# Kernel tuning notes

Measured on AMD Instinct MI355X. Metric: run time of the kernel, lower is better.

The kernel has to match this reference:

```python
import jax, jax.numpy as jnp
import numpy as np

B, N, D = 4, 2048, 256
H, DA, DL = 4, 64, 64          # heads, q/k dim per head, u/v dim per head
NUM_BUCKETS = 128
LN_EPS = 1e-5


def _layernorm(x, g, b):
    mu = jnp.mean(x, axis=-1, keepdims=True)
    var = jnp.var(x, axis=-1, keepdims=True)
    return (x - mu) * jax.lax.rsqrt(var + LN_EPS) * g + b


def setup_inputs() -> dict:
    key = jax.random.key(0)
    ks = jax.random.split(key, 8)
    x = jax.random.normal(ks[0], (B, N, D), jnp.float32)
    lengths = jax.random.randint(ks[1], (B,), 1, N + 1).astype(jnp.int64)
    timestamps = jnp.sort(
        jax.random.randint(ks[2], (B, N), 0, 10_000_000), axis=1
    ).astype(jnp.int64)
    F_uvqk = H * (2 * DL + 2 * DA)
    W_uvqk = jax.random.normal(ks[3], (D, F_uvqk), jnp.float32) * 0.02
    b_uvqk = jnp.zeros((F_uvqk,), jnp.float32)
    W_o = jax.random.normal(ks[4], (H * DL, D), jnp.float32) * 0.02
    b_o = jnp.zeros((D,), jnp.float32)
    ln_in_g = jnp.ones((D,), jnp.float32)
    ln_in_b = jnp.zeros((D,), jnp.float32)
    ln_attn_g = jnp.ones((H * DL,), jnp.float32)
    ln_attn_b = jnp.zeros((H * DL,), jnp.float32)
    w_pos = jax.random.normal(ks[5], (2 * N - 1,), jnp.float32) * 0.02
    w_ts = jax.random.normal(ks[6], (NUM_BUCKETS + 1,), jnp.float32) * 0.02
    return dict(x=x, W_uvqk=W_uvqk, b_uvqk=b_uvqk, W_o=W_o, b_o=b_o,
                ln_in_g=ln_in_g, ln_in_b=ln_in_b,
                ln_attn_g=ln_attn_g, ln_attn_b=ln_attn_b,
                w_pos=w_pos, w_ts=w_ts,
                lengths=lengths, timestamps=timestamps)


def reference(x, W_uvqk, b_uvqk, W_o, b_o, ln_in_g, ln_in_b,
              ln_attn_g, ln_attn_b, w_pos, w_ts, lengths, timestamps):
    # HSTU jagged transduction unit (padded + mask representation).
    nx = _layernorm(x, ln_in_g, ln_in_b)                       # [B,N,D]
    uvqk = jax.nn.silu(nx @ W_uvqk + b_uvqk)                   # fused projection
    u, v, q, k = jnp.split(
        uvqk, [H * DL, 2 * H * DL, 2 * H * DL + H * DA], axis=-1)
    q = q.reshape(B, N, H, DA)
    k = k.reshape(B, N, H, DA)
    v = v.reshape(B, N, H, DL)
    qk = jnp.einsum('bnhd,bmhd->bhnm', q, k)                   # [B,H,N,N]

    # relative position + bucketed relative timestamp bias -> [B,N,N]
    pos = jnp.arange(N)
    pos_bias = w_pos[pos[:, None] - pos[None, :] + (N - 1)]    # [N,N]
    diff = timestamps[:, :, None] - timestamps[:, None, :]     # [B,N,N] int
    bucket = jnp.clip(
        (jnp.log(jnp.maximum(jnp.abs(diff).astype(jnp.float32), 1.0)) / 0.301)
        .astype(jnp.int32), 0, NUM_BUCKETS)
    bias = pos_bias[None] + w_ts[bucket]                       # [B,N,N]

    # non-softmax HSTU attention: silu(scores)/N, causal + valid-key mask
    attn = jax.nn.silu(qk + bias[:, None, :, :]) * (1.0 / N)
    causal = pos[:, None] >= pos[None, :]                      # [N,N]
    valid = pos[None, :] < lengths[:, None]                    # [B,N]
    mask = causal[None, None, :, :] & valid[:, None, None, :]
    attn = jnp.where(mask, attn, 0.0)

    av = jnp.einsum('bhnm,bmhd->bnhd', attn, v).reshape(B, N, H * DL)
    out = (_layernorm(av, ln_attn_g, ln_attn_b) * u) @ W_o + b_o + x
    out = jnp.where(valid[:, :, None], out, 0.0)               # zero padded rows
    return out
```

## Files before the change

### kernel.cpp

```cpp
#include <hip/hip_runtime.h>
#include <stdint.h>

#define BB 4
#define NN 2048
#define DD 256
#define HH 4

typedef __attribute__((ext_vector_type(8))) __bf16 bf16x8;
typedef __attribute__((ext_vector_type(4))) float f32x4;
typedef __attribute__((ext_vector_type(8))) unsigned short u16x8;
typedef __attribute__((ext_vector_type(4))) unsigned short u16x4;

__device__ __forceinline__ unsigned short f2bf(float f) {
  union { float f; uint32_t u; } v; v.f = f;
  uint32_t r = v.u + 0x7fffu + ((v.u >> 16) & 1u);
  return (unsigned short)(r >> 16);
}
__device__ __forceinline__ float bf2f(unsigned short u) {
  union { uint32_t u; float f; } v; v.u = ((uint32_t)u) << 16; return v.f;
}
__device__ __forceinline__ bf16x8 ld8(const unsigned short* p) {
  return __builtin_bit_cast(bf16x8, *(const u16x8*)p);
}
__device__ __forceinline__ f32x4 mfma16(bf16x8 a, bf16x8 b, f32x4 c) {
  return __builtin_amdgcn_mfma_f32_16x16x32_bf16(a, b, c, 0, 0, 0);
}
__device__ __forceinline__ float silu_f(float x) {
  return x / (1.0f + __expf(-x));
}
__device__ __forceinline__ int bias_off(int qt) {
  int a = qt >> 2, r = qt & 3;
  return (a + 1) * (2 * a + r);
}

__global__ __launch_bounds__(256) void k_prep_w(const float* __restrict__ Wu,
                                                const float* __restrict__ Wo,
                                                unsigned short* __restrict__ Wu_t,
                                                unsigned short* __restrict__ Wo_t) {
  __shared__ float T[64][65];
  int bi = blockIdx.x;
  const float* src; unsigned short* dst; int F, f0, d0;
  if (bi < 64) { src = Wu; dst = Wu_t; F = 1024; f0 = (bi >> 2) * 64; d0 = (bi & 3) * 64; }
  else { int j = bi - 64; src = Wo; dst = Wo_t; F = 256; f0 = (j >> 2) * 64; d0 = (j & 3) * 64; }
  int t = threadIdx.x;
  int li = t >> 4;
  int lj = (t & 15) * 4;
  #pragma unroll
  for (int it = 0; it < 4; ++it) {
    int d = li + it * 16;
    float4 v = *(const float4*)(src + (size_t)(d0 + d) * F + f0 + lj);
    T[lj + 0][d] = v.x; T[lj + 1][d] = v.y; T[lj + 2][d] = v.z; T[lj + 3][d] = v.w;
  }
  __syncthreads();
  #pragma unroll
  for (int it = 0; it < 4; ++it) {
    int f = li + it * 16;
    u16x4 o;
    o[0] = f2bf(T[f][lj + 0]); o[1] = f2bf(T[f][lj + 1]);
    o[2] = f2bf(T[f][lj + 2]); o[3] = f2bf(T[f][lj + 3]);
    *(u16x4*)(dst + (size_t)(f0 + f) * 256 + d0 + lj) = o;
  }
}

__global__ __launch_bounds__(256) void k_ln_in(const float* __restrict__ x,
                                               const float* __restrict__ g,
                                               const float* __restrict__ be,
                                               unsigned short* __restrict__ nx) {
  int wave = threadIdx.x >> 6, lane = threadIdx.x & 63;
  int row = blockIdx.x * 4 + wave;
  const float4 v = *(const float4*)(x + (size_t)row * DD + lane * 4);
  float s = v.x + v.y + v.z + v.w;
  float sq = v.x * v.x + v.y * v.y + v.z * v.z + v.w * v.w;
  #pragma unroll
  for (int o = 32; o; o >>= 1) { s += __shfl_xor(s, o); sq += __shfl_xor(sq, o); }
  float mean = s * (1.0f / DD);
  float var = sq * (1.0f / DD) - mean * mean;
  float rstd = rsqrtf(var + 1e-5f);
  const float4 gv = *(const float4*)(g + lane * 4);
  const float4 bv = *(const float4*)(be + lane * 4);
  u16x4 o4;
  o4[0] = f2bf((v.x - mean) * rstd * gv.x + bv.x);
  o4[1] = f2bf((v.y - mean) * rstd * gv.y + bv.y);
  o4[2] = f2bf((v.z - mean) * rstd * gv.z + bv.z);
  o4[3] = f2bf((v.w - mean) * rstd * gv.w + bv.w);
  *(u16x4*)(nx + (size_t)row * DD + lane * 4) = o4;
}

__global__ __launch_bounds__(256) void k_gemm_uvqk(const unsigned short* __restrict__ nx,
                                                   const unsigned short* __restrict__ Wu_t,
                                                   const float* __restrict__ b_uvqk,
                                                   float* __restrict__ u,
                                                   unsigned short* __restrict__ v_tmp,
                                                   unsigned short* __restrict__ q_t,
                                                   unsigned short* __restrict__ k_t) {
  __shared__ unsigned short As[128 * 72];
  __shared__ unsigned short Bs[128 * 72];
  int tid = threadIdx.x, lane = tid & 63, w = tid >> 6;
  int wr = w >> 1, wc = w & 1, c = lane & 15, g = lane >> 4;
  int rblk = blockIdx.x >> 3, cblk = blockIdx.x & 7;
  int R0 = rblk * 128, C0 = cblk * 128;
  f32x4 acc[4][4] = {};
  for (int ks = 0; ks < 4; ++ks) {
    __syncthreads();
    #pragma unroll
    for (int it = 0; it < 4; ++it) {
      int task = tid + it * 256, row = task >> 3, ch = task & 7;
      *(u16x8*)(As + row * 72 + ch * 8) =
          *(const u16x8*)(nx + (size_t)(R0 + row) * 256 + ks * 64 + ch * 8);
      *(u16x8*)(Bs + row * 72 + ch * 8) =
          *(const u16x8*)(Wu_t + (size_t)(C0 + row) * 256 + ks * 64 + ch * 8);
    }
    __syncthreads();
    #pragma unroll
    for (int kk = 0; kk < 2; ++kk) {
      int koff = kk * 32 + g * 8;
      bf16x8 af[4], bfr[4];
      #pragma unroll
      for (int rt = 0; rt < 4; ++rt) af[rt] = ld8(As + (wr * 64 + rt * 16 + c) * 72 + koff);
      #pragma unroll
      for (int ct = 0; ct < 4; ++ct) bfr[ct] = ld8(Bs + (wc * 64 + ct * 16 + c) * 72 + koff);
      #pragma unroll
      for (int rt = 0; rt < 4; ++rt)
        #pragma unroll
        for (int ct = 0; ct < 4; ++ct)
          acc[rt][ct] = mfma16(af[rt], bfr[ct], acc[rt][ct]);
    }
  }
  #pragma unroll
  for (int rt = 0; rt < 4; ++rt) {
    #pragma unroll
    for (int ct = 0; ct < 4; ++ct) {
      int F = C0 + wc * 64 + ct * 16 + c;
      float bb = b_uvqk[F];
      #pragma unroll
      for (int rr = 0; rr < 4; ++rr) {
        int R = R0 + wr * 64 + rt * 16 + g * 4 + rr;
        float pre = acc[rt][ct][rr] + bb;
        float sv = silu_f(pre);
        int b = R >> 11, n = R & 2047;
        if (F < 256) {
          u[(size_t)R * 256 + F] = sv;
        } else if (F < 512) {
          v_tmp[(size_t)R * 256 + (F - 256)] = f2bf(sv);
        } else if (F < 768) {
          int h = (F - 512) >> 6, d = (F - 512) & 63;
          q_t[((size_t)((b << 2) + h) * 2048 + n) * 64 + d] = f2bf(sv);
        } else {
          int h = (F - 768) >> 6, d = (F - 768) & 63;
          k_t[((size_t)((b << 2) + h) * 2048 + n) * 64 + d] = f2bf(sv);
        }
      }
    }
  }
}

__global__ __launch_bounds__(256) void k_vtrans(const unsigned short* __restrict__ v_tmp,
                                                unsigned short* __restrict__ v_t) {
  __shared__ unsigned short T[64 * 72];
  int bi = blockIdx.x;
  int nch = bi & 31, h = (bi >> 5) & 3, b = bi >> 7;
  int n0 = nch * 64;
  int tid = threadIdx.x;
  #pragma unroll
  for (int it = 0; it < 2; ++it) {
    int task = tid + it * 256;
    int i = task >> 3, ch = task & 7;
    *(u16x8*)(T + i * 72 + ch * 8) =
        *(const u16x8*)(v_tmp + ((size_t)(b * 2048 + n0 + i)) * 256 + h * 64 + ch * 8);
  }
  __syncthreads();
  #pragma unroll
  for (int it = 0; it < 2; ++it) {
    int task = tid + it * 256;
    int d = task >> 3, ch = task & 7;
    u16x8 ov;
    #pragma unroll
    for (int uu = 0; uu < 8; ++uu) ov[uu] = T[(ch * 8 + uu) * 72 + d];
    *(u16x8*)(v_t + ((size_t)((b * 4 + h) * 64 + d)) * 2048 + n0 + ch * 8) = ov;
  }
}

__global__ __launch_bounds__(256) void k_bias(const int* __restrict__ ts_raw,
                                              const int* __restrict__ lens_raw,
                                              const float* __restrict__ w_pos,
                                              const float* __restrict__ w_ts,
                                              unsigned short* __restrict__ bias_t) {
  int bi = blockIdx.x;
  int b = bi >> 12, qt = (bi >> 5) & 127, mc = bi & 31;
  if (mc > (qt >> 2)) return;
  int stride = (lens_raw[1] == 0 && lens_raw[3] == 0) ? 2 : 1;
  int Lb = lens_raw[b * stride];
  if (mc * 64 >= Lb) return;
  const int* tsb = ts_raw + (size_t)b * 2048 * stride;
  int t = threadIdx.x;
  int l = t >> 2, mt = t & 3;
  int m = mc * 64 + mt * 16 + (l & 15);
  int nbase = qt * 16 + ((l >> 4) << 2);
  int tm = tsb[m * stride];
  size_t tile = (size_t)(b * 2112 + bias_off(qt) + mc);
  u16x4 o;
  #pragma unroll
  for (int j = 0; j < 4; ++j) {
    int n = nbase + j;
    int dtv = tsb[n * stride] - tm;
    float ad = fmaxf(fabsf((float)dtv), 1.0f);
    int bk = (int)(__log2f(ad) * 2.3028145f);
    bk = bk > 128 ? 128 : bk;
    o[j] = f2bf(w_pos[n - m + 2047] + w_ts[bk]);
  }
  *(u16x4*)(bias_t + tile * 1024 + t * 4) = o;
}

__global__ __launch_bounds__(256) void k_attn(const unsigned short* __restrict__ q_t,
                                              const unsigned short* __restrict__ k_t,
                                              const unsigned short* __restrict__ v_t,
                                              const unsigned short* __restrict__ bias_t,
                                              const int* __restrict__ lens_raw,
                                              float* __restrict__ avP0,
                                              float* __restrict__ avP1) {
  __shared__ unsigned short P_s[4][16 * 72];
  int tid = threadIdx.x, lane = tid & 63, h = tid >> 6;
  int c = lane & 15, g = lane >> 4;
  int bi = blockIdx.x;
  int b, qt, chunk;
  if (bi < 512) { chunk = 0; b = bi & 3; qt = 127 - (bi >> 2); }
  else { chunk = 1; int j = bi - 512; b = j & 3; qt = 127 - (j >> 2); }
  int n0 = qt * 16;
  int stride = (lens_raw[1] == 0 && lens_raw[3] == 0) ? 2 : 1;
  int Lb = lens_raw[b * stride];
  const unsigned short* qp = q_t + (size_t)(b * 4 + h) * 2048 * 64;
  const unsigned short* kp = k_t + (size_t)(b * 4 + h) * 2048 * 64;
  const unsigned short* vp = v_t + (size_t)(b * 4 + h) * 64 * 2048;
  const unsigned short* btile = bias_t + ((size_t)(b * 2112 + bias_off(qt))) * 1024 + lane * 16;

  int m_end = min(n0 + 16, Lb);
  int kv_lo = chunk ? 1024 : 0;
  int kv_hi = chunk ? m_end : min(m_end, 1024);

  bf16x8 qf0 = ld8(qp + (size_t)(n0 + c) * 64 + g * 8);
  bf16x8 qf1 = ld8(qp + (size_t)(n0 + c) * 64 + 32 + g * 8);
  unsigned short* Pw = &P_s[h][0];
  f32x4 av[4] = {};

  for (int m0 = kv_lo; m0 < kv_hi; m0 += 64) {
    const unsigned short* bp = btile + (size_t)(m0 >> 6) * 1024;
    u16x8 bt0 = *(const u16x8*)bp;
    u16x8 bt1 = *(const u16x8*)(bp + 8);
    f32x4 s[4] = {};
    #pragma unroll
    for (int mt = 0; mt < 4; ++mt) {
      const unsigned short* kr = kp + (size_t)(m0 + mt * 16 + c) * 64 + g * 8;
      s[mt] = mfma16(qf0, ld8(kr), s[mt]);
      s[mt] = mfma16(qf1, ld8(kr + 32), s[mt]);
    }
    #pragma unroll
    for (int mt = 0; mt < 4; ++mt) {
      int m = m0 + mt * 16 + c;
      #pragma unroll
      for (int rr = 0; rr < 4; ++rr) {
        int n = n0 + g * 4 + rr;
        int idx = mt * 4 + rr;
        unsigned short ub = idx < 8 ? bt0[idx] : bt1[idx - 8];
        float sv = s[mt][rr] + bf2f(ub);
        float p = (m <= n && m < Lb) ? silu_f(sv) * (1.0f / 2048.0f) : 0.0f;
        Pw[(g * 4 + rr) * 72 + mt * 16 + c] = f2bf(p);
      }
    }
    #pragma unroll
    for (int kk = 0; kk < 2; ++kk) {
      bf16x8 pa = ld8(Pw + c * 72 + kk * 32 + g * 8);
      #pragma unroll
      for (int dt = 0; dt < 4; ++dt) {
        bf16x8 vf = ld8(vp + (size_t)(dt * 16 + c) * 2048 + m0 + kk * 32 + g * 8);
        av[dt] = mfma16(pa, vf, av[dt]);
      }
    }
  }

  if (chunk == 0) {
    #pragma unroll
    for (int dt = 0; dt < 4; ++dt)
      #pragma unroll
      for (int rr = 0; rr < 4; ++rr) {
        int n = n0 + g * 4 + rr;
        avP0[((size_t)(b * 2048 + n)) * 256 + h * 64 + dt * 16 + c] = av[dt][rr];
      }
  } else {
    #pragma unroll
    for (int dt = 0; dt < 4; ++dt)
      #pragma unroll
      for (int rr = 0; rr < 4; ++rr) {
        int n = n0 + g * 4 + rr;
        avP1[((size_t)(b * 1024 + (n - 1024))) * 256 + h * 64 + dt * 16 + c] = av[dt][rr];
      }
  }
}

__global__ __launch_bounds__(256) void k_ln_attn(const float* __restrict__ avP0,
                                                 const float* __restrict__ avP1,
                                                 const float* __restrict__ u,
                                                 const float* __restrict__ g,
                                                 const float* __restrict__ be,
                                                 unsigned short* __restrict__ a2) {
  int wave = threadIdx.x >> 6, lane = threadIdx.x & 63;
  int row = blockIdx.x * 4 + wave;
  int n = row & 2047, b = row >> 11;
  float4 v = *(const float4*)(avP0 + (size_t)row * DD + lane * 4);
  if (n >= 1024) {
    const float4 w = *(const float4*)(avP1 + ((size_t)(b * 1024 + (n - 1024))) * DD + lane * 4);
    v.x += w.x; v.y += w.y; v.z += w.z; v.w += w.w;
  }
  float s = v.x + v.y + v.z + v.w;
  float sq = v.x * v.x + v.y * v.y + v.z * v.z + v.w * v.w;
  #pragma unroll
  for (int o = 32; o; o >>= 1) { s += __shfl_xor(s, o); sq += __shfl_xor(sq, o); }
  float mean = s * (1.0f / DD);
  float var = sq * (1.0f / DD) - mean * mean;
  float rstd = rsqrtf(var + 1e-5f);
  const float4 gv = *(const float4*)(g + lane * 4);
  const float4 bv = *(const float4*)(be + lane * 4);
  const float4 uv = *(const float4*)(u + (size_t)row * DD + lane * 4);
  u16x4 o4;
  o4[0] = f2bf(((v.x - mean) * rstd * gv.x + bv.x) * uv.x);
  o4[1] = f2bf(((v.y - mean) * rstd * gv.y + bv.y) * uv.y);
  o4[2] = f2bf(((v.z - mean) * rstd * gv.z + bv.z) * uv.z);
  o4[3] = f2bf(((v.w - mean) * rstd * gv.w + bv.w) * uv.w);
  *(u16x4*)(a2 + (size_t)row * DD + lane * 4) = o4;
}

__global__ __launch_bounds__(256) void k_gemm_out(const unsigned short* __restrict__ a2,
                                                  const unsigned short* __restrict__ Wo_t,
                                                  const float* __restrict__ b_o,
                                                  const float* __restrict__ x,
                                                  const int* __restrict__ lens_raw,
                                                  float* __restrict__ out) {
  __shared__ unsigned short As[64 * 72];
  __shared__ unsigned short Bs[64 * 72];
  int tid = threadIdx.x, lane = tid & 63, w = tid >> 6;
  int wr = w >> 1, wc = w & 1, c = lane & 15, g = lane >> 4;
  int rblk = blockIdx.x >> 2, cblk = blockIdx.x & 3;
  int R0 = rblk * 64, C0 = cblk * 64;
  int stride = (lens_raw[1] == 0 && lens_raw[3] == 0) ? 2 : 1;
  f32x4 acc[2][2] = {};
  for (int ks = 0; ks < 4; ++ks) {
    __syncthreads();
    #pragma unroll
    for (int it = 0; it < 2; ++it) {
      int task = tid + it * 256, row = task >> 3, ch = task & 7;
      *(u16x8*)(As + row * 72 + ch * 8) =
          *(const u16x8*)(a2 + (size_t)(R0 + row) * 256 + ks * 64 + ch * 8);
      *(u16x8*)(Bs + row * 72 + ch * 8) =
          *(const u16x8*)(Wo_t + (size_t)(C0 + row) * 256 + ks * 64 + ch * 8);
    }
    __syncthreads();
    #pragma unroll
    for (int kk = 0; kk < 2; ++kk) {
      int koff = kk * 32 + g * 8;
      bf16x8 af[2], bfr[2];
      #pragma unroll
      for (int rt = 0; rt < 2; ++rt) af[rt] = ld8(As + (wr * 32 + rt * 16 + c) * 72 + koff);
      #pragma unroll
      for (int ct = 0; ct < 2; ++ct) bfr[ct] = ld8(Bs + (wc * 32 + ct * 16 + c) * 72 + koff);
      #pragma unroll
      for (int rt = 0; rt < 2; ++rt)
        #pragma unroll
        for (int ct = 0; ct < 2; ++ct)
          acc[rt][ct] = mfma16(af[rt], bfr[ct], acc[rt][ct]);
    }
  }
  #pragma unroll
  for (int rt = 0; rt < 2; ++rt) {
    #pragma unroll
    for (int ct = 0; ct < 2; ++ct) {
      int F = C0 + wc * 32 + ct * 16 + c;
      float bo = b_o[F];
      #pragma unroll
      for (int rr = 0; rr < 4; ++rr) {
        int R = R0 + wr * 32 + rt * 16 + g * 4 + rr;
        int b = R >> 11, n = R & 2047;
        int Lb = lens_raw[b * stride];
        float val = acc[rt][ct][rr] + bo + x[(size_t)R * 256 + F];
        out[(size_t)R * 256 + F] = (n < Lb) ? val : 0.0f;
      }
    }
  }
}

extern "C" void kernel_launch(void* const* d_in, const int* in_sizes, int n_in,
                              void* d_out, int out_size, void* d_ws, size_t ws_size,
                              hipStream_t stream) {
  const float* x        = (const float*)d_in[0];
  const float* W_uvqk   = (const float*)d_in[1];
  const float* b_uvqk   = (const float*)d_in[2];
  const float* W_o      = (const float*)d_in[3];
  const float* b_o      = (const float*)d_in[4];
  const float* ln_in_g  = (const float*)d_in[5];
  const float* ln_in_b  = (const float*)d_in[6];
  const float* ln_attn_g= (const float*)d_in[7];
  const float* ln_attn_b= (const float*)d_in[8];
  const float* w_pos    = (const float*)d_in[9];
  const float* w_ts     = (const float*)d_in[10];
  const int*   lengths  = (const int*)d_in[11];
  const int*   tstamps  = (const int*)d_in[12];
  float* out = (float*)d_out;

  char* ws = (char*)d_ws;
  size_t off = 0;
  auto alloc = [&](size_t bytes) -> void* {
    void* p = ws + off;
    off += (bytes + 255) & ~(size_t)255;
    return p;
  };
  unsigned short* Wu_t  = (unsigned short*)alloc(1024 * 256 * 2);
  unsigned short* Wo_t  = (unsigned short*)alloc(256 * 256 * 2);
  unsigned short* nx    = (unsigned short*)alloc((size_t)8192 * 256 * 2);
  float*          u     = (float*)alloc((size_t)8192 * 256 * 4);
  unsigned short* v_t   = (unsigned short*)alloc((size_t)8192 * 256 * 2);
  unsigned short* q_t   = (unsigned short*)alloc((size_t)8192 * 256 * 2);
  unsigned short* k_t   = (unsigned short*)alloc((size_t)8192 * 256 * 2);
  float*          avP0  = (float*)alloc((size_t)8192 * 256 * 4);
  unsigned short* a2    = (unsigned short*)alloc((size_t)8192 * 256 * 2);
  unsigned short* v_tmp = (unsigned short*)alloc((size_t)8192 * 256 * 2);
  unsigned short* bias_t = (unsigned short*)v_tmp;
  (void)alloc((size_t)4 * 2112 * 1024 * 2 - (size_t)8192 * 256 * 2);
  float*          avP1  = (float*)nx;

  k_prep_w<<<80, 256, 0, stream>>>(W_uvqk, W_o, Wu_t, Wo_t);
  k_ln_in<<<2048, 256, 0, stream>>>(x, ln_in_g, ln_in_b, nx);
  k_gemm_uvqk<<<512, 256, 0, stream>>>(nx, Wu_t, b_uvqk, u, v_tmp, q_t, k_t);
  k_vtrans<<<512, 256, 0, stream>>>(v_tmp, v_t);
  k_bias<<<16384, 256, 0, stream>>>(tstamps, lengths, w_pos, w_ts, bias_t);
  k_attn<<<768, 256, 0, stream>>>(q_t, k_t, v_t, bias_t, lengths, avP0, avP1);
  k_ln_attn<<<2048, 256, 0, stream>>>(avP0, avP1, u, ln_attn_g, ln_attn_b, a2);
  k_gemm_out<<<512, 256, 0, stream>>>(a2, Wo_t, b_o, x, lengths, out);
}
```

Baseline: 221.5 us.

## Split attention KV range into 256-wide chunks with atomic accumulation

Attention work is now split into eight KV chunks of 256 keys per query tile instead of two fixed halves. Blocks whose chunk lies entirely beyond the causal or length limit exit early. Partial results are combined with float atomicAdd into a buffer that a new kernel zeroes first, and the layernorm kernel reads that single buffer. This aims to balance the triangular workload across more blocks, at the cost of atomic traffic, nondeterministic summation order and an extra zeroing launch.

```diff
diff --git a/kernel.cpp b/kernel.cpp
--- a/kernel.cpp
+++ b/kernel.cpp
@@ -60,6 +60,12 @@
     o[2] = f2bf(T[f][lj + 2]); o[3] = f2bf(T[f][lj + 3]);
     *(u16x4*)(dst + (size_t)(f0 + f) * 256 + d0 + lj) = o;
   }
+}
+
+__global__ __launch_bounds__(256) void k_zero(float* __restrict__ p) {
+  size_t i = ((size_t)blockIdx.x * 256 + threadIdx.x) * 4;
+  float4 z = {0.0f, 0.0f, 0.0f, 0.0f};
+  *(float4*)(p + i) = z;
 }
 
 __global__ __launch_bounds__(256) void k_ln_in(const float* __restrict__ x,
@@ -216,26 +222,24 @@
                                               const unsigned short* __restrict__ v_t,
                                               const unsigned short* __restrict__ bias_t,
                                               const int* __restrict__ lens_raw,
-                                              float* __restrict__ avP0,
-                                              float* __restrict__ avP1) {
+                                              float* __restrict__ avF) {
   __shared__ unsigned short P_s[4][16 * 72];
   int tid = threadIdx.x, lane = tid & 63, h = tid >> 6;
   int c = lane & 15, g = lane >> 4;
   int bi = blockIdx.x;
-  int b, qt, chunk;
-  if (bi < 512) { chunk = 0; b = bi & 3; qt = 127 - (bi >> 2); }
-  else { chunk = 1; int j = bi - 512; b = j & 3; qt = 127 - (j >> 2); }
+  int b = bi & 3, qt = 127 - ((bi >> 2) & 127), ck = bi >> 9;
   int n0 = qt * 16;
   int stride = (lens_raw[1] == 0 && lens_raw[3] == 0) ? 2 : 1;
   int Lb = lens_raw[b * stride];
+  int m_end = min(n0 + 16, Lb);
+  int kv_lo = ck * 256;
+  if (kv_lo >= m_end) return;
+  int kv_hi = min(kv_lo + 256, m_end);
+
   const unsigned short* qp = q_t + (size_t)(b * 4 + h) * 2048 * 64;
   const unsigned short* kp = k_t + (size_t)(b * 4 + h) * 2048 * 64;
   const unsigned short* vp = v_t + (size_t)(b * 4 + h) * 64 * 2048;
   const unsigned short* btile = bias_t + ((size_t)(b * 2112 + bias_off(qt))) * 1024 + lane * 16;
-
-  int m_end = min(n0 + 16, Lb);
-  int kv_lo = chunk ? 1024 : 0;
-  int kv_hi = chunk ? m_end : min(m_end, 1024);
 
   bf16x8 qf0 = ld8(qp + (size_t)(n0 + c) * 64 + g * 8);
   bf16x8 qf1 = ld8(qp + (size_t)(n0 + c) * 64 + 32 + g * 8);
@@ -277,39 +281,23 @@
     }
   }
 
-  if (chunk == 0) {
-    #pragma unroll
-    for (int dt = 0; dt < 4; ++dt)
-      #pragma unroll
-      for (int rr = 0; rr < 4; ++rr) {
-        int n = n0 + g * 4 + rr;
-        avP0[((size_t)(b * 2048 + n)) * 256 + h * 64 + dt * 16 + c] = av[dt][rr];
-      }
-  } else {
-    #pragma unroll
-    for (int dt = 0; dt < 4; ++dt)
-      #pragma unroll
-      for (int rr = 0; rr < 4; ++rr) {
-        int n = n0 + g * 4 + rr;
-        avP1[((size_t)(b * 1024 + (n - 1024))) * 256 + h * 64 + dt * 16 + c] = av[dt][rr];
-      }
-  }
-}
-
-__global__ __launch_bounds__(256) void k_ln_attn(const float* __restrict__ avP0,
-                                                 const float* __restrict__ avP1,
+  #pragma unroll
+  for (int dt = 0; dt < 4; ++dt)
+    #pragma unroll
+    for (int rr = 0; rr < 4; ++rr) {
+      int n = n0 + g * 4 + rr;
+      atomicAdd(avF + ((size_t)(b * 2048 + n)) * 256 + h * 64 + dt * 16 + c, av[dt][rr]);
+    }
+}
+
+__global__ __launch_bounds__(256) void k_ln_attn(const float* __restrict__ avF,
                                                  const float* __restrict__ u,
                                                  const float* __restrict__ g,
                                                  const float* __restrict__ be,
                                                  unsigned short* __restrict__ a2) {
   int wave = threadIdx.x >> 6, lane = threadIdx.x & 63;
   int row = blockIdx.x * 4 + wave;
-  int n = row & 2047, b = row >> 11;
-  float4 v = *(const float4*)(avP0 + (size_t)row * DD + lane * 4);
-  if (n >= 1024) {
-    const float4 w = *(const float4*)(avP1 + ((size_t)(b * 1024 + (n - 1024))) * DD + lane * 4);
-    v.x += w.x; v.y += w.y; v.z += w.z; v.w += w.w;
-  }
+  const float4 v = *(const float4*)(avF + (size_t)row * DD + lane * 4);
   float s = v.x + v.y + v.z + v.w;
   float sq = v.x * v.x + v.y * v.y + v.z * v.z + v.w * v.w;
   #pragma unroll
@@ -418,19 +406,19 @@
   unsigned short* v_t   = (unsigned short*)alloc((size_t)8192 * 256 * 2);
   unsigned short* q_t   = (unsigned short*)alloc((size_t)8192 * 256 * 2);
   unsigned short* k_t   = (unsigned short*)alloc((size_t)8192 * 256 * 2);
-  float*          avP0  = (float*)alloc((size_t)8192 * 256 * 4);
+  float*          avF   = (float*)alloc((size_t)8192 * 256 * 4);
   unsigned short* a2    = (unsigned short*)alloc((size_t)8192 * 256 * 2);
   unsigned short* v_tmp = (unsigned short*)alloc((size_t)8192 * 256 * 2);
   unsigned short* bias_t = (unsigned short*)v_tmp;
   (void)alloc((size_t)4 * 2112 * 1024 * 2 - (size_t)8192 * 256 * 2);
-  float*          avP1  = (float*)nx;
-
+
+  k_zero<<<2048, 256, 0, stream>>>(avF);
   k_prep_w<<<80, 256, 0, stream>>>(W_uvqk, W_o, Wu_t, Wo_t);
   k_ln_in<<<2048, 256, 0, stream>>>(x, ln_in_g, ln_in_b, nx);
   k_gemm_uvqk<<<512, 256, 0, stream>>>(nx, Wu_t, b_uvqk, u, v_tmp, q_t, k_t);
   k_vtrans<<<512, 256, 0, stream>>>(v_tmp, v_t);
   k_bias<<<16384, 256, 0, stream>>>(tstamps, lengths, w_pos, w_ts, bias_t);
-  k_attn<<<768, 256, 0, stream>>>(q_t, k_t, v_t, bias_t, lengths, avP0, avP1);
-  k_ln_attn<<<2048, 256, 0, stream>>>(avP0, avP1, u, ln_attn_g, ln_attn_b, a2);
+  k_attn<<<4096, 256, 0, stream>>>(q_t, k_t, v_t, bias_t, lengths, avF);
+  k_ln_attn<<<2048, 256, 0, stream>>>(avF, u, ln_attn_g, ln_attn_b, a2);
   k_gemm_out<<<512, 256, 0, stream>>>(a2, Wo_t, b_o, x, lengths, out);
 }
```

Result: faster. 216.4 us (-2.3%).
